# Kernel tuning notes

Measured on AMD Instinct MI355X. Metric: run time of the kernel, lower is better.

Reference implementation:

```python
import jax, jax.numpy as jnp
import numpy as np
from jax import lax

NEG = -1000.0  # torch.full((N,S), -1000.0) init in dp_align


def setup_inputs() -> dict:
    key = jax.random.key(0)
    ks = jax.random.split(key, 4)
    N, S, h = 128, 2048, 256          # nodes, segments, hsize
    d = 2 * h                         # bi-LSTM output dim = 2*hsize
    seg_text_feats = jax.random.normal(ks[0], (N, d), jnp.float32)
    vid_feature = jax.random.normal(ks[1], (S, d), jnp.float32)
    # relation_query: Linear(4h, h) -> ReLU -> (Dropout, eval=identity) -> Linear(h, 1)
    W1 = jax.random.normal(ks[2], (h, 2 * d), jnp.float32) / np.sqrt(2.0 * d)
    b1 = jnp.zeros((h,), jnp.float32)
    W2 = jax.random.normal(ks[3], (1, h), jnp.float32) / np.sqrt(float(h))
    b2 = jnp.zeros((1,), jnp.float32)
    return {"seg_text_feats": seg_text_feats, "vid_feature": vid_feature,
            "W1": W1, "b1": b1, "W2": W2, "b2": b2}


def reference(seg_text_feats, vid_feature, W1, b1, W2, b2):
    N, d = seg_text_feats.shape
    S = vid_feature.shape[0]
    # Pairwise MLP logits for every (node, segment) cell, vectorized:
    # concat(text, vid) @ W1^T == text @ W1[:, :d]^T + vid @ W1[:, d:]^T
    A = seg_text_feats @ W1[:, :d].T           # [N, h]
    B = vid_feature @ W1[:, d:].T              # [S, h]
    H = jax.nn.relu(A[:, None, :] + B[None, :, :] + b1)   # [N, S, h]
    logits = jnp.einsum('nsh,h->ns', H, W2[0]) + b2[0]     # [N, S]
    logsig = jax.nn.log_sigmoid(logits)

    n_idx = jnp.arange(N)
    # DP over columns, right to left. prev_col is arr[:, s+1] (virtual col S = NEG).
    def step(prev_col, s):
        ls = logsig[:, s]
        nxt = jnp.concatenate([prev_col[1:], jnp.full((1,), NEG, prev_col.dtype)])  # arr[n+1, s+1]
        curr = ls + jnp.where(n_idx == N - 1, 0.0, nxt)   # last node: no chain term
        take = curr >= prev_col                            # tie -> take current (matches >=)
        val = jnp.where(take, curr, prev_col)
        in_range = (s >= n_idx) & (s <= S - N + n_idx)     # start_ind/end_ind bands
        col = jnp.where(in_range, val, NEG)
        return col, take

    _, takes = lax.scan(step, jnp.full((N,), NEG), jnp.arange(S - 1, -1, -1))
    take_curr = takes[::-1].T                              # [N, S]

    # Backtrack parent pointers from (node 0, segment 0).
    def walk(carry, s):
        n, align = carry
        nc = jnp.minimum(n, N - 1)
        tc = take_curr[nc, s] & (n < N)
        align = align.at[nc].set(jnp.where(tc, s, align[nc]))
        return (n + tc.astype(jnp.int32), align), None

    (_, align), _ = lax.scan(walk, (jnp.int32(0), jnp.zeros((N,), jnp.int32)), jnp.arange(S))

    aggregated_logits = jnp.mean(logits[n_idx, align])     # sum(logit)/num_nodes
    adj_matrix = jnp.zeros((N + S, N + S), jnp.float32).at[S + n_idx, align].set(1.0)
    return adj_matrix, aggregated_logits
```

## Files before the change

### kernel.cpp

```cpp
#include <hip/hip_runtime.h>
#include <math.h>

#define NEGC (-1000.0f)

__global__ __launch_bounds__(256) void kzero_adj(float4* __restrict__ out4) {
    const int i = blockIdx.x * 256 + threadIdx.x;
    if (i < 1183744) out4[i] = make_float4(0.f, 0.f, 0.f, 0.f);
}

__global__ __launch_bounds__(256) void k1_gemm(
    const float* __restrict__ seg, const float* __restrict__ vid,
    const float* __restrict__ W1, const float* __restrict__ b1,
    float* __restrict__ A2, float* __restrict__ B2)
{
    __shared__ float Xs[32][64];
    __shared__ float Ws[32][64];
    const int tid = threadIdx.x;
    const int tx = tid & 15, ty = tid >> 4;
    const int lr = tid >> 2;
    const int lk = (tid & 3) * 8;
    const int colBase = blockIdx.x * 64;
    const int rowBase = blockIdx.y * 64;
    const bool isSeg = (rowBase < 128);
    const float* __restrict__ X = isSeg ? seg : vid;
    const int xRow = isSeg ? rowBase : (rowBase - 128);
    const int wOff = isSeg ? 0 : 512;

    float acc[4][4] = {};

    for (int k0 = 0; k0 < 512; k0 += 32) {
        const float* xp = X + (size_t)(xRow + lr) * 512 + (k0 + lk);
        const float4 xa = *(const float4*)xp;
        const float4 xb = *(const float4*)(xp + 4);
        const float* wp = W1 + (size_t)(colBase + lr) * 1024 + (wOff + k0 + lk);
        const float4 wa = *(const float4*)wp;
        const float4 wb = *(const float4*)(wp + 4);
        __syncthreads();
        Xs[lk + 0][lr] = xa.x; Xs[lk + 1][lr] = xa.y;
        Xs[lk + 2][lr] = xa.z; Xs[lk + 3][lr] = xa.w;
        Xs[lk + 4][lr] = xb.x; Xs[lk + 5][lr] = xb.y;
        Xs[lk + 6][lr] = xb.z; Xs[lk + 7][lr] = xb.w;
        Ws[lk + 0][lr] = wa.x; Ws[lk + 1][lr] = wa.y;
        Ws[lk + 2][lr] = wa.z; Ws[lk + 3][lr] = wa.w;
        Ws[lk + 4][lr] = wb.x; Ws[lk + 5][lr] = wb.y;
        Ws[lk + 6][lr] = wb.z; Ws[lk + 7][lr] = wb.w;
        __syncthreads();
        #pragma unroll
        for (int kk = 0; kk < 32; ++kk) {
            const float4 a4 = *(const float4*)&Xs[kk][4 * ty];
            const float4 b4 = *(const float4*)&Ws[kk][4 * tx];
            const float* a = (const float*)&a4;
            const float* b = (const float*)&b4;
            #pragma unroll
            for (int i = 0; i < 4; ++i)
                #pragma unroll
                for (int j = 0; j < 4; ++j)
                    acc[i][j] = fmaf(a[i], b[j], acc[i][j]);
        }
    }

    float* __restrict__ outp = (isSeg ? A2 : B2) + (size_t)xRow * 256;
    const int c = colBase + 4 * tx;
    #pragma unroll
    for (int i = 0; i < 4; ++i) {
        float4 v = make_float4(acc[i][0], acc[i][1], acc[i][2], acc[i][3]);
        if (isSeg) {
            v.x += b1[c + 0]; v.y += b1[c + 1]; v.z += b1[c + 2]; v.w += b1[c + 3];
        }
        *(float4*)(outp + (size_t)(4 * ty + i) * 256 + c) = v;
    }
}

__global__ __launch_bounds__(256) void k2_logits(
    const float* __restrict__ A2, const float* __restrict__ B2,
    const float* __restrict__ W2, const float* __restrict__ b2p,
    float* __restrict__ logitsT, float* __restrict__ lsT)
{
    __shared__ float As[32][64];
    __shared__ float Bs[32][64];
    __shared__ float w2s[256];
    const int tid = threadIdx.x;
    const int tx = tid & 15, ty = tid >> 4;
    const int lr = tid >> 2;
    const int lk = (tid & 3) * 8;
    const int nBase = blockIdx.x * 64;
    const int sBase = blockIdx.y * 64;
    w2s[tid] = W2[tid];
    const float b2v = b2p[0];

    float acc[4][4] = {};

    for (int k0 = 0; k0 < 256; k0 += 32) {
        const float* ap = A2 + (size_t)(nBase + lr) * 256 + (k0 + lk);
        const float4 aa = *(const float4*)ap;
        const float4 ab = *(const float4*)(ap + 4);
        const float* bp = B2 + (size_t)(sBase + lr) * 256 + (k0 + lk);
        const float4 ba = *(const float4*)bp;
        const float4 bb = *(const float4*)(bp + 4);
        __syncthreads();
        As[lk + 0][lr] = aa.x; As[lk + 1][lr] = aa.y;
        As[lk + 2][lr] = aa.z; As[lk + 3][lr] = aa.w;
        As[lk + 4][lr] = ab.x; As[lk + 5][lr] = ab.y;
        As[lk + 6][lr] = ab.z; As[lk + 7][lr] = ab.w;
        Bs[lk + 0][lr] = ba.x; Bs[lk + 1][lr] = ba.y;
        Bs[lk + 2][lr] = ba.z; Bs[lk + 3][lr] = ba.w;
        Bs[lk + 4][lr] = bb.x; Bs[lk + 5][lr] = bb.y;
        Bs[lk + 6][lr] = bb.z; Bs[lk + 7][lr] = bb.w;
        __syncthreads();
        #pragma unroll
        for (int kk = 0; kk < 32; ++kk) {
            const float w = w2s[k0 + kk];
            const float4 a4 = *(const float4*)&As[kk][4 * ty];
            const float4 b4 = *(const float4*)&Bs[kk][4 * tx];
            const float* a = (const float*)&a4;
            const float* b = (const float*)&b4;
            #pragma unroll
            for (int i = 0; i < 4; ++i)
                #pragma unroll
                for (int j = 0; j < 4; ++j)
                    acc[i][j] = fmaf(fmaxf(a[i] + b[j], 0.0f), w, acc[i][j]);
        }
    }

    const int nb = nBase + 4 * ty;
    #pragma unroll
    for (int j = 0; j < 4; ++j) {
        const int s = sBase + 4 * tx + j;
        float4 lg, ls;
        float* lgp = (float*)&lg;
        float* lsp = (float*)&ls;
        #pragma unroll
        for (int i = 0; i < 4; ++i) {
            const float x = acc[i][j] + b2v;
            lgp[i] = x;
            lsp[i] = fminf(x, 0.0f) - log1pf(expf(-fabsf(x)));
        }
        *(float4*)&logitsT[(size_t)s * 128 + nb] = lg;
        *(float4*)&lsT[(size_t)s * 128 + nb] = ls;
    }
}

__global__ __launch_bounds__(64) void k3_dp(
    const float* __restrict__ lsT, const float* __restrict__ logitsT,
    float* __restrict__ out)
{
    __shared__ unsigned takeW[128 * 65];
    __shared__ int alignSh[128];
    const int lane = threadIdx.x;
    const int n0 = 2 * lane, n1 = n0 + 1;
    const bool isLast = (lane == 63);
    const float2* __restrict__ ls2 = (const float2*)lsT;

    float p0 = NEGC, p1 = NEGC;
    unsigned u0 = 2047u - (unsigned)n0;
    unsigned u1 = u0 - 1u;
    unsigned w0 = 0u, w1 = 0u;

    auto step = [&](float2 lsv) {
        float nxt1 = __int_as_float(__builtin_amdgcn_update_dpp(
            0, __float_as_int(p0), 0x130 , 0xf, 0xf, true));
        nxt1 = isLast ? 0.0f : nxt1;
        const float c0 = lsv.x + p1;
        const float c1 = lsv.y + nxt1;
        const unsigned t0 = (c0 >= p0) ? 1u : 0u;
        const unsigned t1 = (c1 >= p1) ? 1u : 0u;
        const float v0 = fmaxf(c0, p0);
        const float v1 = fmaxf(c1, p1);
        p0 = (u0 <= 1920u) ? v0 : NEGC;
        p1 = (u1 <= 1920u) ? v1 : NEGC;
        --u0; --u1;
        w0 = (w0 << 1) | t0;
        w1 = (w1 << 1) | t1;
    };

    float2 bufA[16], bufB[16];
    #pragma unroll
    for (int j = 0; j < 16; ++j) bufA[j] = ls2[(2047 - j) * 64 + lane];

    int wIdx = 63;
    for (int g = 0; g < 128; g += 2) {
        #pragma unroll
        for (int j = 0; j < 16; ++j) bufB[j] = ls2[(2047 - 16 * (g + 1) - j) * 64 + lane];
        #pragma unroll
        for (int j = 0; j < 16; ++j) step(bufA[j]);
        if (g + 2 < 128) {
            #pragma unroll
            for (int j = 0; j < 16; ++j) bufA[j] = ls2[(2047 - 16 * (g + 2) - j) * 64 + lane];
        }
        #pragma unroll
        for (int j = 0; j < 16; ++j) step(bufB[j]);
        takeW[n0 * 65 + wIdx] = w0;
        takeW[n1 * 65 + wIdx] = w1;
        w0 = 0u; w1 = 0u;
        --wIdx;
    }

    alignSh[n0] = 0;
    alignSh[n1] = 0;
    __syncthreads();

    if (lane == 0) {
        int pos = 0;
        for (int n = 0; n < 128; ++n) {
            const unsigned* row = &takeW[n * 65];
            int wi = pos >> 5;
            unsigned w = (pos < 2048) ? (row[wi] & (0xFFFFFFFFu << (pos & 31))) : 0u;
            while (w == 0u) {
                ++wi;
                if (wi >= 64) break;
                w = row[wi];
            }
            if (w == 0u) break;
            const int found = wi * 32 + __builtin_ctz(w);
            alignSh[n] = found;
            pos = found + 1;
        }
    }
    __syncthreads();

    const int a0 = alignSh[n0];
    const int a1 = alignSh[n1];
    out[(size_t)(2048 + n0) * 2176 + a0] = 1.0f;
    out[(size_t)(2048 + n1) * 2176 + a1] = 1.0f;
    float sum = logitsT[(size_t)a0 * 128 + n0] + logitsT[(size_t)a1 * 128 + n1];
    #pragma unroll
    for (int off = 32; off >= 1; off >>= 1) sum += __shfl_down(sum, off);
    if (lane == 0) out[(size_t)2176 * 2176] = sum * (1.0f / 128.0f);
}

extern "C" void kernel_launch(void* const* d_in, const int* in_sizes, int n_in,
                              void* d_out, int out_size, void* d_ws, size_t ws_size,
                              hipStream_t stream)
{
    const float* seg = (const float*)d_in[0];
    const float* vid = (const float*)d_in[1];
    const float* W1  = (const float*)d_in[2];
    const float* b1  = (const float*)d_in[3];
    const float* W2  = (const float*)d_in[4];
    const float* b2  = (const float*)d_in[5];
    float* out = (float*)d_out;
    float* ws  = (float*)d_ws;

    float* A2      = ws;
    float* B2      = ws + 32768;
    float* logitsT = ws + 557056;
    float* lsT     = ws + 819200;

    kzero_adj<<<dim3(4624), dim3(256), 0, stream>>>((float4*)out);
    k1_gemm<<<dim3(4, 34), dim3(256), 0, stream>>>(seg, vid, W1, b1, A2, B2);
    k2_logits<<<dim3(2, 32), dim3(256), 0, stream>>>(A2, B2, W2, b2, logitsT, lsT);
    k3_dp<<<dim3(1), dim3(64), 0, stream>>>(lsT, logitsT, out);
}
```

Before: 237.2 us.

## Fuse adjacency zeroing into GEMM, trim DP step with inline asm, parallelize backtrack

The separate zero-fill kernel is folded into the GEMM launch as extra blocks, which removes one kernel launch. The serial DP inner step is rewritten in inline assembly: the take bit is shifted into the mask with add-with-carry, and the band masking only runs in the edge column groups where it can apply. The backtrack now uses a wave-wide ballot over the 64 words of each row instead of a single-lane scan. The masking logic is replaced by a reset of the u counters and an edge-only check, and dropping the last-lane zeroing relies on DPP bound_ctrl returning 0. Both assumptions carry correctness risk.

```diff
diff --git a/kernel.cpp b/kernel.cpp
--- a/kernel.cpp
+++ b/kernel.cpp
@@ -3,24 +3,24 @@
 
 #define NEGC (-1000.0f)
 
-__global__ __launch_bounds__(256) void kzero_adj(float4* __restrict__ out4) {
-    const int i = blockIdx.x * 256 + threadIdx.x;
-    if (i < 1183744) out4[i] = make_float4(0.f, 0.f, 0.f, 0.f);
-}
-
-__global__ __launch_bounds__(256) void k1_gemm(
+__global__ __launch_bounds__(256) void k1z_gemm(
     const float* __restrict__ seg, const float* __restrict__ vid,
     const float* __restrict__ W1, const float* __restrict__ b1,
-    float* __restrict__ A2, float* __restrict__ B2)
-{
+    float* __restrict__ A2, float* __restrict__ B2, float4* __restrict__ out4)
+{
+    if (blockIdx.x >= 136) {
+        const int i = (blockIdx.x - 136) * 256 + threadIdx.x;
+        if (i < 1183744) out4[i] = make_float4(0.f, 0.f, 0.f, 0.f);
+        return;
+    }
     __shared__ float Xs[32][64];
     __shared__ float Ws[32][64];
     const int tid = threadIdx.x;
     const int tx = tid & 15, ty = tid >> 4;
     const int lr = tid >> 2;
     const int lk = (tid & 3) * 8;
-    const int colBase = blockIdx.x * 64;
-    const int rowBase = blockIdx.y * 64;
+    const int colBase = (blockIdx.x & 3) * 64;
+    const int rowBase = (blockIdx.x >> 2) * 64;
     const bool isSeg = (rowBase < 128);
     const float* __restrict__ X = isSeg ? seg : vid;
     const int xRow = isSeg ? rowBase : (rowBase - 128);
@@ -148,7 +148,6 @@
     __shared__ int alignSh[128];
     const int lane = threadIdx.x;
     const int n0 = 2 * lane, n1 = n0 + 1;
-    const bool isLast = (lane == 63);
     const float2* __restrict__ ls2 = (const float2*)lsT;
 
     float p0 = NEGC, p1 = NEGC;
@@ -156,21 +155,36 @@
     unsigned u1 = u0 - 1u;
     unsigned w0 = 0u, w1 = 0u;
 
-    auto step = [&](float2 lsv) {
+    auto core = [&](float lx, float ly, float nx) {
+        float c0, c1;
+        unsigned long long cc;
+        asm volatile(
+            "v_add_f32 %[c0], %[lx], %[p1]\n\t"
+            "v_add_f32 %[c1], %[ly], %[nx]\n\t"
+            "v_cmp_ge_f32 vcc, %[c0], %[p0]\n\t"
+            "v_cmp_ge_f32 %[cc], %[c1], %[p1]\n\t"
+            "v_addc_co_u32 %[w0], vcc, %[w0], %[w0], vcc\n\t"
+            "v_addc_co_u32 %[w1], %[cc], %[w1], %[w1], %[cc]\n\t"
+            "v_max_f32 %[p0], %[c0], %[p0]\n\t"
+            "v_max_f32 %[p1], %[c1], %[p1]\n\t"
+            : [p0]"+v"(p0), [p1]"+v"(p1), [w0]"+v"(w0), [w1]"+v"(w1),
+              [c0]"=&v"(c0), [c1]"=&v"(c1), [cc]"=&s"(cc)
+            : [lx]"v"(lx), [ly]"v"(ly), [nx]"v"(nx)
+            : "vcc");
+    };
+
+    auto stepF = [&](float2 lsv) {
         float nxt1 = __int_as_float(__builtin_amdgcn_update_dpp(
             0, __float_as_int(p0), 0x130 , 0xf, 0xf, true));
-        nxt1 = isLast ? 0.0f : nxt1;
-        const float c0 = lsv.x + p1;
-        const float c1 = lsv.y + nxt1;
-        const unsigned t0 = (c0 >= p0) ? 1u : 0u;
-        const unsigned t1 = (c1 >= p1) ? 1u : 0u;
-        const float v0 = fmaxf(c0, p0);
-        const float v1 = fmaxf(c1, p1);
-        p0 = (u0 <= 1920u) ? v0 : NEGC;
-        p1 = (u1 <= 1920u) ? v1 : NEGC;
+        core(lsv.x, lsv.y, nxt1);
+    };
+    auto stepM = [&](float2 lsv) {
+        float nxt1 = __int_as_float(__builtin_amdgcn_update_dpp(
+            0, __float_as_int(p0), 0x130, 0xf, 0xf, true));
+        core(lsv.x, lsv.y, nxt1);
+        p0 = (u0 <= 1920u) ? p0 : NEGC;
+        p1 = (u1 <= 1920u) ? p1 : NEGC;
         --u0; --u1;
-        w0 = (w0 << 1) | t0;
-        w1 = (w1 << 1) | t1;
     };
 
     float2 bufA[16], bufB[16];
@@ -179,16 +193,31 @@
 
     int wIdx = 63;
     for (int g = 0; g < 128; g += 2) {
+        if (wIdx == 3) {
+            u0 = (unsigned)(127 - n0);
+            u1 = (unsigned)(127 - n1);
+        }
+        const bool masked = (wIdx >= 60) || (wIdx <= 3);
         #pragma unroll
         for (int j = 0; j < 16; ++j) bufB[j] = ls2[(2047 - 16 * (g + 1) - j) * 64 + lane];
-        #pragma unroll
-        for (int j = 0; j < 16; ++j) step(bufA[j]);
+        if (masked) {
+            #pragma unroll
+            for (int j = 0; j < 16; ++j) stepM(bufA[j]);
+        } else {
+            #pragma unroll
+            for (int j = 0; j < 16; ++j) stepF(bufA[j]);
+        }
         if (g + 2 < 128) {
             #pragma unroll
             for (int j = 0; j < 16; ++j) bufA[j] = ls2[(2047 - 16 * (g + 2) - j) * 64 + lane];
         }
-        #pragma unroll
-        for (int j = 0; j < 16; ++j) step(bufB[j]);
+        if (masked) {
+            #pragma unroll
+            for (int j = 0; j < 16; ++j) stepM(bufB[j]);
+        } else {
+            #pragma unroll
+            for (int j = 0; j < 16; ++j) stepF(bufB[j]);
+        }
         takeW[n0 * 65 + wIdx] = w0;
         takeW[n1 * 65 + wIdx] = w1;
         w0 = 0u; w1 = 0u;
@@ -199,22 +228,19 @@
     alignSh[n1] = 0;
     __syncthreads();
 
-    if (lane == 0) {
-        int pos = 0;
-        for (int n = 0; n < 128; ++n) {
-            const unsigned* row = &takeW[n * 65];
-            int wi = pos >> 5;
-            unsigned w = (pos < 2048) ? (row[wi] & (0xFFFFFFFFu << (pos & 31))) : 0u;
-            while (w == 0u) {
-                ++wi;
-                if (wi >= 64) break;
-                w = row[wi];
-            }
-            if (w == 0u) break;
-            const int found = wi * 32 + __builtin_ctz(w);
-            alignSh[n] = found;
-            pos = found + 1;
-        }
+    int pos = 0;
+    for (int n = 0; n < 128; ++n) {
+        unsigned w = takeW[n * 65 + lane];
+        const int wi0 = pos >> 5;
+        if (lane < wi0) w = 0u;
+        else if (lane == wi0) w &= (0xFFFFFFFFu << (pos & 31));
+        const unsigned long long m = __ballot(w != 0u);
+        if (m == 0ull) break;
+        const int fl = __builtin_ctzll(m);
+        const unsigned fw = (unsigned)__builtin_amdgcn_readlane((int)w, fl);
+        const int s = fl * 32 + __builtin_ctz(fw);
+        if (lane == 0) alignSh[n] = s;
+        pos = s + 1;
     }
     __syncthreads();
 
@@ -246,8 +272,7 @@
     float* logitsT = ws + 557056;
     float* lsT     = ws + 819200;
 
-    kzero_adj<<<dim3(4624), dim3(256), 0, stream>>>((float4*)out);
-    k1_gemm<<<dim3(4, 34), dim3(256), 0, stream>>>(seg, vid, W1, b1, A2, B2);
+    k1z_gemm<<<dim3(4760), dim3(256), 0, stream>>>(seg, vid, W1, b1, A2, B2, (float4*)out);
     k2_logits<<<dim3(2, 32), dim3(256), 0, stream>>>(A2, B2, W2, b2, logitsT, lsT);
     k3_dp<<<dim3(1), dim3(64), 0, stream>>>(lsT, logitsT, out);
 }
```

Result: faster. 210.2 us (-11.4%).
